# Kernel optimization log

Measured on AMD Instinct MI355X. Metric: run time of the kernel, lower is better.

## Reference

```python
import jax, jax.numpy as jnp
import numpy as np

FIX_SCALE = np.array([[0.,0.,0.],[1.,0.,0.],[0.,1.,0.],[0.,0.,1.],[-1.,0.,0.],[0.,-1.,0.]], dtype=np.float32)
NUM_HEADS = 8
ATTN_DIMS = 512
HEAD_DIMS = ATTN_DIMS // NUM_HEADS
NUM_LEARN = 6
SIG_CLAMP = 9.21  # safe_sigmoid clamp


def quat_to_rotmat(q):
    # q: [G,4] (w,x,y,z), normalized -> [G,3,3]
    q = q / jnp.linalg.norm(q, axis=-1, keepdims=True)
    w, x, y, z = q[..., 0], q[..., 1], q[..., 2], q[..., 3]
    r0 = jnp.stack([1 - 2*(y*y + z*z), 2*(x*y - w*z), 2*(x*z + w*y)], -1)
    r1 = jnp.stack([2*(x*y + w*z), 1 - 2*(x*x + z*z), 2*(y*z - w*x)], -1)
    r2 = jnp.stack([2*(x*z - w*y), 2*(y*z + w*x), 1 - 2*(x*x + y*y)], -1)
    return jnp.stack([r0, r1, r2], -2)


def bilinear_sample(fm, gx, gy):
    # fm: [C,H,W]; gx,gy: [...] in [-1,1]; align_corners=False, zero padding
    C, H, W = fm.shape
    x = (gx + 1.0) * (W * 0.5) - 0.5
    y = (gy + 1.0) * (H * 0.5) - 0.5
    x0 = jnp.floor(x); y0 = jnp.floor(y)
    wx1 = x - x0; wx0 = 1.0 - wx1
    wy1 = y - y0; wy0 = 1.0 - wy1

    def gather(xf, yf):
        xi = xf.astype(jnp.int32); yi = yf.astype(jnp.int32)
        valid = (xi >= 0) & (xi < W) & (yi >= 0) & (yi < H)
        xi = jnp.clip(xi, 0, W - 1); yi = jnp.clip(yi, 0, H - 1)
        return fm[:, yi, xi] * valid[None].astype(fm.dtype)  # [C, ...]

    out = (gather(x0, y0) * (wx0 * wy0)[None]
           + gather(x0 + 1, y0) * (wx1 * wy0)[None]
           + gather(x0, y0 + 1) * (wx0 * wy1)[None]
           + gather(x0 + 1, y0 + 1) * (wx1 * wy1)[None])
    return jnp.moveaxis(out, 0, -1)  # [..., C]


def setup_inputs() -> dict:
    key = jax.random.key(0)
    ks = jax.random.split(key, 16)
    G, BS, GFD = 8192, 1, 32
    means = jax.random.uniform(ks[0], (G, 3), minval=-1.0, maxval=1.0)
    means = means.at[:, 2].add(3.0)  # push in front of camera
    scales = jax.random.uniform(ks[1], (G, 3), minval=0.01, maxval=0.1)
    rotations = jax.random.normal(ks[2], (G, 4))
    features = jax.random.normal(ks[3], (BS, G, 3, GFD))
    transforms = jnp.tile(jnp.eye(4)[None], (G, 1, 1)) + 0.01 * jax.random.normal(ks[4], (G, 4, 4))
    f = 64.0
    proj = jnp.array([[f, 0., 32., 0.], [0., f, 32., 0.], [0., 0., 1., 0.], [0., 0., 0., 1.]], dtype=jnp.float32)
    projection = jnp.tile(proj[None], (BS, 1, 1))
    image_features = jax.random.normal(ks[5], (BS, 256, 64, 64))
    s = lambda d: 1.0 / np.sqrt(d)
    Wq = jax.random.normal(ks[6], (GFD, ATTN_DIMS)) * s(GFD)
    Wk = jax.random.normal(ks[7], (ATTN_DIMS, 256)) * s(256)
    Wv = jax.random.normal(ks[8], (ATTN_DIMS, 256)) * s(256)
    W_off = jax.random.normal(ks[9], (HEAD_DIMS + 3, NUM_LEARN * 3)) * s(HEAD_DIMS + 3)
    b_off = jnp.zeros((NUM_LEARN * 3,))
    Wout = jax.random.normal(ks[10], (ATTN_DIMS, GFD)) * s(ATTN_DIMS)
    b_out = jnp.zeros((GFD,))
    return {"means": means, "scales": scales, "rotations": rotations, "features": features,
            "transforms": transforms, "projection": projection, "image_features": image_features,
            "Wq": Wq, "Wk": Wk, "Wv": Wv, "W_off": W_off, "b_off": b_off, "Wout": Wout, "b_out": b_out}


def reference(means, scales, rotations, features, transforms, projection, image_features,
              Wq, Wk, Wv, W_off, b_off, Wout, b_out):
    G = means.shape[0]
    bs = features.shape[0]
    H, HD = NUM_HEADS, HEAD_DIMS
    h_img, w_img = image_features.shape[-2:]

    # queries: [bs,G,3,attn] -> [bs,H,G,3,hd]
    q_full = jnp.einsum('bgtf,fa->bgta', features, Wq)
    q = q_full.reshape(bs, G, 3, H, HD).transpose(0, 3, 1, 2, 4)

    # transform means to world space with per-gaussian 4x4
    homo = jnp.concatenate([means, jnp.ones((G, 1), means.dtype)], -1)  # [G,4]
    means_w = jnp.einsum('gij,gj->gi', transforms, homo)[:, :3]  # [G,3]

    # OffsetNet: per-head learnable offsets from (world mean, token-mean query)
    q_mean = q.mean(axis=3)  # [bs,H,G,hd]
    m_b = jnp.broadcast_to(means_w[None, None], (bs, H, G, 3))
    off_in = jnp.concatenate([m_b, q_mean], -1)  # [bs,H,G,hd+3]
    learnable = jax.nn.sigmoid(jnp.clip(off_in @ W_off + b_off, -SIG_CLAMP, SIG_CLAMP))
    learnable = learnable.reshape(bs, H, G, NUM_LEARN, 3) - 0.5
    fix = jnp.broadcast_to(jnp.asarray(FIX_SCALE)[None, None, None], (bs, H, G, FIX_SCALE.shape[0], 3))
    scale_all = jnp.concatenate([fix, learnable], axis=-2)  # [bs,H,G,K,3]
    K = scale_all.shape[-2]

    offset_pts = scale_all * scales[None, None, :, None, :]
    RT = jnp.swapaxes(quat_to_rotmat(rotations), -1, -2)  # [G,3,3]
    offset_pts = jnp.einsum('gij,bhgkj->bhgki', RT, offset_pts) + means_w[None, None, :, None, :]

    # project to 2D, normalize to [0,1), then to grid coords [-1,1]
    pts4 = jnp.concatenate([offset_pts, jnp.ones_like(offset_pts[..., :1])], -1)
    p = jnp.einsum('bij,bhgkj->bhgki', projection, pts4)
    p2 = p[..., :2] / jnp.clip(p[..., 2:3], 1e-5)
    wh = jnp.array([w_img, h_img], dtype=p2.dtype)
    pnorm = jnp.clip(p2 / wh, 0.0, 0.9999)
    grid = 2.0 * pnorm - 1.0  # [bs,H,G,K,2]

    # key/value maps via 1x1 conv, split into per-head channel groups
    kmap = jnp.einsum('ac,bchw->bahw', Wk, image_features).reshape(bs, H, HD, h_img, w_img)
    vmap_ = jnp.einsum('ac,bchw->bahw', Wv, image_features).reshape(bs, H, HD, h_img, w_img)

    sample_bh = jax.vmap(jax.vmap(bilinear_sample, in_axes=(0, 0, 0)), in_axes=(0, 0, 0))
    k_s = sample_bh(kmap, grid[..., 0], grid[..., 1])   # [bs,H,G,K,hd]
    v_s = sample_bh(vmap_, grid[..., 0], grid[..., 1])  # [bs,H,G,K,hd]

    scale = HD ** -0.5
    scores = jnp.einsum('bhgid,bhgkd->bhgik', q, k_s) * scale
    attn = jax.nn.softmax(scores, axis=-1)
    out = jnp.einsum('bhgik,bhgkd->bhgid', attn, v_s)  # [bs,H,G,3,hd]
    out = out.transpose(0, 2, 3, 1, 4).reshape(bs, G, 3, H * HD)  # b g i (h d)
    out = out @ Wout + b_out
    return out + features
```

## Files before the change

kernel.cpp:

```cpp
#include <hip/hip_runtime.h>
#include <hip/hip_bf16.h>

typedef __hip_bfloat16 bf16;
typedef __attribute__((ext_vector_type(8))) short short8;
typedef __attribute__((ext_vector_type(4))) float float4v;

__device__ __forceinline__ unsigned short f2bfu(float f) {
    bf16 b = __float2bfloat16(f);
    return *(unsigned short*)&b;
}
__device__ __forceinline__ void ld8bf(const bf16* p, float* f) {
    uint4 u = *(const uint4*)p;
    f[0] = __uint_as_float(u.x << 16); f[1] = __uint_as_float(u.x & 0xffff0000u);
    f[2] = __uint_as_float(u.y << 16); f[3] = __uint_as_float(u.y & 0xffff0000u);
    f[4] = __uint_as_float(u.z << 16); f[5] = __uint_as_float(u.z & 0xffff0000u);
    f[6] = __uint_as_float(u.w << 16); f[7] = __uint_as_float(u.w & 0xffff0000u);
}
__device__ __forceinline__ unsigned packbf(float lo, float hi) {
    return (unsigned)f2bfu(lo) | ((unsigned)f2bfu(hi) << 16);
}

__global__ __launch_bounds__(256) void preconvert_kernel(
    const float* __restrict__ img, const float* __restrict__ Wk,
    const float* __restrict__ Wv, unsigned short* __restrict__ imgbf,
    unsigned short* __restrict__ wkvbf)
{
    const size_t base = ((size_t)blockIdx.x * 256 + threadIdx.x) * 4;
    float4 v;
    unsigned short* dst;
    if (base < 1048576) {
        v = *(const float4*)(img + base);
        dst = imgbf + base;
    } else {
        size_t o = base - 1048576;
        v = *(const float4*)((o < 131072) ? (Wk + o) : (Wv + (o - 131072)));
        dst = wkvbf + o;
    }
    *(uint2*)dst = make_uint2(packbf(v.x, v.y), packbf(v.z, v.w));
}

__global__ __launch_bounds__(256) void conv_bf16_kernel(
    const unsigned short* __restrict__ imgbf, const unsigned short* __restrict__ wkvbf,
    bf16* __restrict__ buf)
{
    __shared__ __attribute__((aligned(16))) unsigned short Bt[64][264];
    const int tid = threadIdx.x;
    const int p0 = blockIdx.x * 64;
    const int o0 = blockIdx.y * 64;

#pragma unroll
    for (int i = 0; i < 4; i++) {
        int chunk = i * 256 + tid;
        int kp  = chunk >> 3;
        int pxg = (chunk & 7) * 8;
        uint4 r0 = *(const uint4*)(imgbf + (size_t)(2 * kp) * 4096 + p0 + pxg);
        uint4 r1 = *(const uint4*)(imgbf + (size_t)(2 * kp + 1) * 4096 + p0 + pxg);
        unsigned lo[8], hi[8];
        lo[0] = r0.x & 0xffffu; lo[1] = r0.x >> 16; lo[2] = r0.y & 0xffffu; lo[3] = r0.y >> 16;
        lo[4] = r0.z & 0xffffu; lo[5] = r0.z >> 16; lo[6] = r0.w & 0xffffu; lo[7] = r0.w >> 16;
        hi[0] = r1.x & 0xffffu; hi[1] = r1.x >> 16; hi[2] = r1.y & 0xffffu; hi[3] = r1.y >> 16;
        hi[4] = r1.z & 0xffffu; hi[5] = r1.z >> 16; hi[6] = r1.w & 0xffffu; hi[7] = r1.w >> 16;
#pragma unroll
        for (int j = 0; j < 8; j++)
            *(unsigned*)&Bt[pxg + j][2 * kp] = lo[j] | (hi[j] << 16);
    }
    __syncthreads();

    const int w = tid >> 6, l = tid & 63;
    const int m = l & 15, quad = l >> 4;
    const int mrow = w * 16 + m;
    const unsigned short* Wsel = wkvbf + ((o0 < 512) ? 0 : 131072);
    const int obase = (o0 < 512) ? o0 : (o0 - 512);

    float4v acc[4] = {{0,0,0,0},{0,0,0,0},{0,0,0,0},{0,0,0,0}};
#pragma unroll
    for (int kk = 0; kk < 8; kk++) {
        const int kofs = kk * 32 + quad * 8;
        short8 af = *(const short8*)&Bt[mrow][kofs];
#pragma unroll
        for (int nt = 0; nt < 4; nt++) {
            const int row = obase + nt * 16 + m;
            short8 b8 = *(const short8*)(Wsel + (size_t)row * 256 + kofs);
            acc[nt] = __builtin_amdgcn_mfma_f32_16x16x32_bf16(af, b8, acc[nt], 0, 0, 0);
        }
    }
#pragma unroll
    for (int nt = 0; nt < 4; nt++) {
#pragma unroll
        for (int r = 0; r < 4; r++) {
            size_t px = p0 + w * 16 + quad * 4 + r;
            buf[px * 1024 + o0 + nt * 16 + m] = __float2bfloat16(acc[nt][r]);
        }
    }
}

__global__ __launch_bounds__(256) void conv_mfma_kernel(
    const float* __restrict__ img, const float* __restrict__ Wk,
    const float* __restrict__ Wv, bf16* __restrict__ buf)
{
    __shared__ __attribute__((aligned(16))) unsigned short Bt[64][264];
    const int tid = threadIdx.x;
    const int p0 = blockIdx.x * 64;
    const int o0 = blockIdx.y * 64;

#pragma unroll
    for (int i = 0; i < 4; i++) {
        int chunk = i * 256 + tid;
        int kp  = chunk >> 3;
        int pxg = (chunk & 7) * 8;
        const float* r0 = img + (size_t)(2 * kp) * 4096 + p0 + pxg;
        const float* r1 = img + (size_t)(2 * kp + 1) * 4096 + p0 + pxg;
        float4 a0 = *(const float4*)r0, a1 = *(const float4*)(r0 + 4);
        float4 b0 = *(const float4*)r1, b1 = *(const float4*)(r1 + 4);
        unsigned lo[8], hi[8];
        lo[0] = f2bfu(a0.x); lo[1] = f2bfu(a0.y); lo[2] = f2bfu(a0.z); lo[3] = f2bfu(a0.w);
        lo[4] = f2bfu(a1.x); lo[5] = f2bfu(a1.y); lo[6] = f2bfu(a1.z); lo[7] = f2bfu(a1.w);
        hi[0] = f2bfu(b0.x); hi[1] = f2bfu(b0.y); hi[2] = f2bfu(b0.z); hi[3] = f2bfu(b0.w);
        hi[4] = f2bfu(b1.x); hi[5] = f2bfu(b1.y); hi[6] = f2bfu(b1.z); hi[7] = f2bfu(b1.w);
#pragma unroll
        for (int j = 0; j < 8; j++)
            *(unsigned*)&Bt[pxg + j][2 * kp] = lo[j] | (hi[j] << 16);
    }
    __syncthreads();

    const int w = tid >> 6, l = tid & 63;
    const int m = l & 15, quad = l >> 4;
    const int mrow = w * 16 + m;
    const float* Wsel = (o0 < 512) ? Wk : Wv;
    const int obase = (o0 < 512) ? o0 : (o0 - 512);

    float4v acc[4] = {{0,0,0,0},{0,0,0,0},{0,0,0,0},{0,0,0,0}};
#pragma unroll
    for (int kk = 0; kk < 8; kk++) {
        const int kofs = kk * 32 + quad * 8;
        short8 af = *(const short8*)&Bt[mrow][kofs];
#pragma unroll
        for (int nt = 0; nt < 4; nt++) {
            const int row = obase + nt * 16 + m;
            const float* wp = Wsel + (size_t)row * 256 + kofs;
            float4 w0 = *(const float4*)wp, w1 = *(const float4*)(wp + 4);
            short8 b8;
            b8[0] = (short)f2bfu(w0.x); b8[1] = (short)f2bfu(w0.y);
            b8[2] = (short)f2bfu(w0.z); b8[3] = (short)f2bfu(w0.w);
            b8[4] = (short)f2bfu(w1.x); b8[5] = (short)f2bfu(w1.y);
            b8[6] = (short)f2bfu(w1.z); b8[7] = (short)f2bfu(w1.w);
            acc[nt] = __builtin_amdgcn_mfma_f32_16x16x32_bf16(af, b8, acc[nt], 0, 0, 0);
        }
    }
#pragma unroll
    for (int nt = 0; nt < 4; nt++) {
#pragma unroll
        for (int r = 0; r < 4; r++) {
            size_t px = p0 + w * 16 + quad * 4 + r;
            buf[px * 1024 + o0 + nt * 16 + m] = __float2bfloat16(acc[nt][r]);
        }
    }
}

__global__ __launch_bounds__(256) void qgemm_kernel(
    const float* __restrict__ features, const float* __restrict__ Wq,
    bf16* __restrict__ qfull)
{
    __shared__ __attribute__((aligned(16))) unsigned short WqT[256][40];
    const int tid = threadIdx.x;
    const int R0 = blockIdx.x * 64;
    const int n0 = blockIdx.y * 256;
#pragma unroll
    for (int k = 0; k < 32; k++)
        WqT[tid][k] = f2bfu(Wq[(size_t)k * 512 + n0 + tid]);
    __syncthreads();

    const int w = tid >> 6, l = tid & 63, m = l & 15, quad = l >> 4;
    const int row = R0 + w * 16 + m;
    const float* fp = features + (size_t)row * 32 + quad * 8;
    float4 f0 = *(const float4*)fp, f1 = *(const float4*)(fp + 4);
    short8 af;
    af[0] = (short)f2bfu(f0.x); af[1] = (short)f2bfu(f0.y);
    af[2] = (short)f2bfu(f0.z); af[3] = (short)f2bfu(f0.w);
    af[4] = (short)f2bfu(f1.x); af[5] = (short)f2bfu(f1.y);
    af[6] = (short)f2bfu(f1.z); af[7] = (short)f2bfu(f1.w);
    float4v acc[16];
#pragma unroll
    for (int t = 0; t < 16; t++) acc[t] = (float4v){0.f, 0.f, 0.f, 0.f};
#pragma unroll
    for (int t = 0; t < 16; t++) {
        short8 b8 = *(const short8*)&WqT[t * 16 + m][quad * 8];
        acc[t] = __builtin_amdgcn_mfma_f32_16x16x32_bf16(af, b8, acc[t], 0, 0, 0);
    }
    const int rb = R0 + w * 16 + quad * 4;
#pragma unroll
    for (int t = 0; t < 16; t++)
#pragma unroll
        for (int r = 0; r < 4; r++)
            qfull[(size_t)(rb + r) * 512 + n0 + t * 16 + m] = __float2bfloat16(acc[t][r]);
}

__global__ __launch_bounds__(256, 7) void attn_core_kernel(
    const float* __restrict__ means, const float* __restrict__ scales,
    const float* __restrict__ rot,   const float* __restrict__ transforms,
    const float* __restrict__ projection, const float* __restrict__ W_off,
    const float* __restrict__ b_off, const bf16* __restrict__ buf,
    bf16* __restrict__ qfull)
{
    __shared__ __attribute__((aligned(16))) float qf[1536];
    __shared__ __attribute__((aligned(16))) unsigned short vsh[6144];
    __shared__ __attribute__((aligned(16))) float qm_u[512];
    __shared__ float lrn[144];
    __shared__ float mw[3], sc3[3], Rt[9], pr[12];

    short4* corner = (short4*)qm_u;
    float*  att    = qm_u + 192;
    float*  wofl   = (float*)vsh;
    float*  bofl   = wofl + 1206;

    const int g = blockIdx.x, tid = threadIdx.x;

    for (int i = tid; i < 1206; i += 256) wofl[i] = W_off[i];
    if (tid < 18) bofl[tid] = b_off[tid];
    if (tid >= 32 && tid < 35) {
        sc3[tid - 32] = scales[(size_t)g * 3 + (tid - 32)];
    } else if (tid >= 36 && tid < 48) {
        pr[tid - 36] = projection[tid - 36];
    } else if (tid == 48) {
        float w = rot[(size_t)g * 4],     x = rot[(size_t)g * 4 + 1];
        float y = rot[(size_t)g * 4 + 2], z = rot[(size_t)g * 4 + 3];
        float n = rsqrtf(w * w + x * x + y * y + z * z);
        w *= n; x *= n; y *= n; z *= n;
        float R00 = 1 - 2 * (y * y + z * z), R01 = 2 * (x * y - w * z), R02 = 2 * (x * z + w * y);
        float R10 = 2 * (x * y + w * z), R11 = 1 - 2 * (x * x + z * z), R12 = 2 * (y * z - w * x);
        float R20 = 2 * (x * z - w * y), R21 = 2 * (y * z + w * x), R22 = 1 - 2 * (x * x + y * y);
        Rt[0] = R00; Rt[1] = R10; Rt[2] = R20;
        Rt[3] = R01; Rt[4] = R11; Rt[5] = R21;
        Rt[6] = R02; Rt[7] = R12; Rt[8] = R22;
    } else if (tid >= 52 && tid < 55) {
        int i = tid - 52;
        float m0 = means[(size_t)g * 3];
        float m1 = means[(size_t)g * 3 + 1];
        float m2 = means[(size_t)g * 3 + 2];
        const float* T = transforms + (size_t)g * 16 + i * 4;
        mw[i] = T[0] * m0 + T[1] * m1 + T[2] * m2 + T[3];
    }
    {
        const unsigned* qsrc = (const unsigned*)((const unsigned short*)qfull + (size_t)g * 1536);
#pragma unroll
        for (int i = 0; i < 3; i++) {
            int e = tid + i * 256;
            unsigned u = qsrc[e];
            qf[e * 2]     = __uint_as_float(u << 16);
            qf[e * 2 + 1] = __uint_as_float(u & 0xffff0000u);
        }
    }
    __syncthreads();

    qm_u[tid]       = (qf[tid]       + qf[tid + 512] + qf[tid + 1024]) * (1.f / 3.f);
    qm_u[tid + 256] = (qf[tid + 256] + qf[tid + 768] + qf[tid + 1280]) * (1.f / 3.f);
    __syncthreads();

    if (tid < 144) {
        int h = tid / 18, l = tid % 18;
        float s = bofl[l];
#pragma unroll
        for (int i = 0; i < 3; i++) s += mw[i] * wofl[i * 18 + l];
        for (int d = 0; d < 64; d++) s += qm_u[h * 64 + d] * wofl[(3 + d) * 18 + l];
        s = fminf(fmaxf(s, -9.21f), 9.21f);
        lrn[tid] = 1.f / (1.f + expf(-s)) - 0.5f;
    }
    __syncthreads();

    if (tid < 96) {
        int h = tid / 12, k = tid % 12;
        float s0, s1, s2;
        if (k < 6) {
            const float FSx[6] = {0.f, 1.f, 0.f, 0.f, -1.f, 0.f};
            const float FSy[6] = {0.f, 0.f, 1.f, 0.f, 0.f, -1.f};
            const float FSz[6] = {0.f, 0.f, 0.f, 1.f, 0.f, 0.f};
            s0 = FSx[k]; s1 = FSy[k]; s2 = FSz[k];
        } else {
            int b = h * 18 + (k - 6) * 3;
            s0 = lrn[b]; s1 = lrn[b + 1]; s2 = lrn[b + 2];
        }
        float o0 = s0 * sc3[0], o1 = s1 * sc3[1], o2 = s2 * sc3[2];
        float wx = Rt[0] * o0 + Rt[1] * o1 + Rt[2] * o2 + mw[0];
        float wy = Rt[3] * o0 + Rt[4] * o1 + Rt[5] * o2 + mw[1];
        float wz = Rt[6] * o0 + Rt[7] * o1 + Rt[8] * o2 + mw[2];
        float px = pr[0] * wx + pr[1] * wy + pr[2]  * wz + pr[3];
        float py = pr[4] * wx + pr[5] * wy + pr[6]  * wz + pr[7];
        float pz = pr[8] * wx + pr[9] * wy + pr[10] * wz + pr[11];
        pz = fmaxf(pz, 1e-5f);
        float gx = fminf(fmaxf(px / pz * (1.f / 64.f), 0.f), 0.9999f);
        float gy = fminf(fmaxf(py / pz * (1.f / 64.f), 0.f), 0.9999f);
        float x = gx * 64.f - 0.5f, y = gy * 64.f - 0.5f;
        float fx = floorf(x), fy = floorf(y);
        short4 cn;
        cn.x = (short)(int)fx;
        cn.y = (short)(int)fy;
        cn.z = (short)(unsigned short)fminf((x - fx) * 65536.f, 65535.f);
        cn.w = (short)(unsigned short)fminf((y - fy) * 65536.f, 65535.f);
        corner[tid] = cn;
    }
    __syncthreads();

    {
        const int slice = tid & 7, d0 = slice * 8, grp = tid >> 3;
#pragma unroll
        for (int it = 0; it < 3; it++) {
            const int p = it * 32 + grp;
            const int h = p / 12, k = p - h * 12;
            short4 cn = corner[p];
            int x0 = cn.x, y0 = cn.y, x1 = x0 + 1, y1 = y0 + 1;
            float wx1 = (float)(unsigned short)cn.z * (1.f / 65536.f);
            float wy1 = (float)(unsigned short)cn.w * (1.f / 65536.f);
            float wx0 = 1.f - wx1, wy0 = 1.f - wy1;
            bool vx0 = (unsigned)x0 < 64u, vx1 = (unsigned)x1 < 64u;
            bool vy0 = (unsigned)y0 < 64u, vy1 = (unsigned)y1 < 64u;
            int xc0 = min(max(x0, 0), 63), xc1 = min(max(x1, 0), 63);
            int yc0 = min(max(y0, 0), 63), yc1 = min(max(y1, 0), 63);
            int   off[4];
            float wt[4];
            off[0] = (yc0 * 64 + xc0) * 1024; wt[0] = (vx0 & vy0) ? wx0 * wy0 : 0.f;
            off[1] = (yc0 * 64 + xc1) * 1024; wt[1] = (vx1 & vy0) ? wx1 * wy0 : 0.f;
            off[2] = (yc1 * 64 + xc0) * 1024; wt[2] = (vx0 & vy1) ? wx0 * wy1 : 0.f;
            off[3] = (yc1 * 64 + xc1) * 1024; wt[3] = (vx1 & vy1) ? wx1 * wy1 : 0.f;
            const int a = h * 64 + d0;
            const bf16* bp = buf + a;
            float ka[8] = {0,0,0,0,0,0,0,0}, va[8] = {0,0,0,0,0,0,0,0}, t8[8];
#pragma unroll
            for (int c = 0; c < 4; c++) {
                const float w = wt[c];
                ld8bf(bp + off[c], t8);
#pragma unroll
                for (int j = 0; j < 8; j++) ka[j] += w * t8[j];
                ld8bf(bp + off[c] + 512, t8);
#pragma unroll
                for (int j = 0; j < 8; j++) va[j] += w * t8[j];
            }
            uint4 pv;
            pv.x = packbf(va[0], va[1]); pv.y = packbf(va[2], va[3]);
            pv.z = packbf(va[4], va[5]); pv.w = packbf(va[6], va[7]);
            *(uint4*)(vsh + p * 64 + d0) = pv;
            float sp[3];
#pragma unroll
            for (int t = 0; t < 3; t++) {
                const float* qp = qf + t * 512 + a;
                float s = 0.f;
#pragma unroll
                for (int j = 0; j < 8; j++) s += qp[j] * ka[j];
                sp[t] = s;
            }
#pragma unroll
            for (int msk = 1; msk < 8; msk <<= 1) {
#pragma unroll
                for (int t = 0; t < 3; t++) sp[t] += __shfl_xor(sp[t], msk);
            }
            if (slice == 0) {
#pragma unroll
                for (int t = 0; t < 3; t++) att[(h * 3 + t) * 12 + k] = sp[t] * 0.125f;
            }
        }
    }
    __syncthreads();

    if (tid < 24) {
        float* row = att + tid * 12;
        float m = row[0];
#pragma unroll
        for (int k = 1; k < 12; k++) m = fmaxf(m, row[k]);
        float e_[12]; float ssum = 0.f;
#pragma unroll
        for (int k = 0; k < 12; k++) { e_[k] = expf(row[k] - m); ssum += e_[k]; }
        float inv = 1.f / ssum;
#pragma unroll
        for (int k = 0; k < 12; k++) row[k] = e_[k] * inv;
    }
    __syncthreads();

    {
        unsigned* oa32 = (unsigned*)((unsigned short*)qfull + (size_t)g * 1536);
#pragma unroll
        for (int i = 0; i < 3; i++) {
            int e = tid + i * 256;
            int t = e >> 8, a2 = (e & 255) * 2;
            int h = a2 >> 6, dd = a2 & 63;
            const float* ar = att + (h * 3 + t) * 12;
            const unsigned short* vp = vsh + (h * 12) * 64 + dd;
            float s0 = 0.f, s1 = 0.f;
#pragma unroll
            for (int k = 0; k < 12; k++) {
                unsigned u = *(const unsigned*)(vp + k * 64);
                s0 += ar[k] * __uint_as_float(u << 16);
                s1 += ar[k] * __uint_as_float(u & 0xffff0000u);
            }
            oa32[e] = packbf(s0, s1);
        }
    }
}

__global__ __launch_bounds__(256) void outgemm_kernel(
    const bf16* __restrict__ oa, const float* __restrict__ Wout,
    const float* __restrict__ b_out, const float* __restrict__ features,
    float* __restrict__ out)
{
    __shared__ __attribute__((aligned(16))) unsigned short WT[32][520];
    const int tid = threadIdx.x;
    const int R0 = blockIdx.x * 64;
#pragma unroll
    for (int j = 0; j < 64; j++) {
        int lin = j * 256 + tid;
        WT[lin & 31][lin >> 5] = f2bfu(Wout[lin]);
    }
    __syncthreads();

    const int w = tid >> 6, l = tid & 63, m = l & 15, quad = l >> 4;
    const int row = R0 + w * 16 + m;
    float4v acc[2] = {{0,0,0,0},{0,0,0,0}};
#pragma unroll
    for (int kk = 0; kk < 16; kk++) {
        short8 af = *(const short8*)((const unsigned short*)oa + (size_t)row * 512 + kk * 32 + quad * 8);
#pragma unroll
        for (int t = 0; t < 2; t++) {
            short8 b8 = *(const short8*)&WT[t * 16 + m][kk * 32 + quad * 8];
            acc[t] = __builtin_amdgcn_mfma_f32_16x16x32_bf16(af, b8, acc[t], 0, 0, 0);
        }
    }
    const int rb = R0 + w * 16 + quad * 4;
#pragma unroll
    for (int t = 0; t < 2; t++) {
        int col = t * 16 + m;
        float bb = b_out[col];
#pragma unroll
        for (int r = 0; r < 4; r++) {
            int rr = rb + r;
            out[(size_t)rr * 32 + col] = acc[t][r] + bb + features[(size_t)rr * 32 + col];
        }
    }
}

__global__ __launch_bounds__(256, 6) void attn_fused_kernel(
    const float* __restrict__ means, const float* __restrict__ scales,
    const float* __restrict__ rot,   const float* __restrict__ features,
    const float* __restrict__ transforms, const float* __restrict__ projection,
    const float* __restrict__ Wq,    const float* __restrict__ W_off,
    const float* __restrict__ b_off, const float* __restrict__ Wout,
    const float* __restrict__ b_out, const bf16* __restrict__ buf,
    float* __restrict__ out)
{
    __shared__ float feat[96];
    __shared__ __attribute__((aligned(16))) float qf[1536];
    __shared__ float qm[512];
    __shared__ float mw[3], sc3[3], Rt[9], pr[12];
    __shared__ float lrn[144];
    __shared__ int   coff[96][4];
    __shared__ float cwt[96][4];
    __shared__ __attribute__((aligned(16))) char pool[12288];
    __shared__ float att[288];

    unsigned short* vsh = (unsigned short*)pool;
    const int g = blockIdx.x, tid = threadIdx.x;

    if (tid < 96) {
        feat[tid] = features[(size_t)g * 96 + tid];
    } else if (tid < 99) {
        sc3[tid - 96] = scales[(size_t)g * 3 + (tid - 96)];
    } else if (tid >= 100 && tid < 112) {
        pr[tid - 100] = projection[tid - 100];
    } else if (tid == 112) {
        float w = rot[(size_t)g * 4],     x = rot[(size_t)g * 4 + 1];
        float y = rot[(size_t)g * 4 + 2], z = rot[(size_t)g * 4 + 3];
        float n = rsqrtf(w * w + x * x + y * y + z * z);
        w *= n; x *= n; y *= n; z *= n;
        float R00 = 1 - 2 * (y * y + z * z), R01 = 2 * (x * y - w * z), R02 = 2 * (x * z + w * y);
        float R10 = 2 * (x * y + w * z), R11 = 1 - 2 * (x * x + z * z), R12 = 2 * (y * z - w * x);
        float R20 = 2 * (x * z - w * y), R21 = 2 * (y * z + w * x), R22 = 1 - 2 * (x * x + y * y);
        Rt[0] = R00; Rt[1] = R10; Rt[2] = R20;
        Rt[3] = R01; Rt[4] = R11; Rt[5] = R21;
        Rt[6] = R02; Rt[7] = R12; Rt[8] = R22;
    } else if (tid >= 116 && tid < 119) {
        int i = tid - 116;
        float m0 = means[(size_t)g * 3];
        float m1 = means[(size_t)g * 3 + 1];
        float m2 = means[(size_t)g * 3 + 2];
        const float* T = transforms + (size_t)g * 16 + i * 4;
        mw[i] = T[0] * m0 + T[1] * m1 + T[2] * m2 + T[3];
    }
    __syncthreads();

    {
        const int a0 = tid * 2;
        float s00 = 0.f, s01 = 0.f, s10 = 0.f, s11 = 0.f, s20 = 0.f, s21 = 0.f;
#pragma unroll
        for (int f = 0; f < 32; f++) {
            float2 w2 = *(const float2*)(Wq + (size_t)f * 512 + a0);
            float f0 = feat[f], f1 = feat[32 + f], f2 = feat[64 + f];
            s00 += f0 * w2.x; s01 += f0 * w2.y;
            s10 += f1 * w2.x; s11 += f1 * w2.y;
            s20 += f2 * w2.x; s21 += f2 * w2.y;
        }
        *(float2*)(qf + a0)        = make_float2(s00, s01);
        *(float2*)(qf + 512 + a0)  = make_float2(s10, s11);
        *(float2*)(qf + 1024 + a0) = make_float2(s20, s21);
    }
    __syncthreads();

    qm[tid]       = (qf[tid]       + qf[tid + 512] + qf[tid + 1024]) * (1.f / 3.f);
    qm[tid + 256] = (qf[tid + 256] + qf[tid + 768] + qf[tid + 1280]) * (1.f / 3.f);
    __syncthreads();

    if (tid < 144) {
        int h = tid / 18, l = tid % 18;
        float s = b_off[l];
#pragma unroll
        for (int i = 0; i < 3; i++) s += mw[i] * W_off[i * 18 + l];
        for (int d = 0; d < 64; d++) s += qm[h * 64 + d] * W_off[(size_t)(3 + d) * 18 + l];
        s = fminf(fmaxf(s, -9.21f), 9.21f);
        lrn[tid] = 1.f / (1.f + expf(-s)) - 0.5f;
    }
    __syncthreads();

    if (tid < 96) {
        int h = tid / 12, k = tid % 12;
        float s0, s1, s2;
        if (k < 6) {
            const float FSx[6] = {0.f, 1.f, 0.f, 0.f, -1.f, 0.f};
            const float FSy[6] = {0.f, 0.f, 1.f, 0.f, 0.f, -1.f};
            const float FSz[6] = {0.f, 0.f, 0.f, 1.f, 0.f, 0.f};
            s0 = FSx[k]; s1 = FSy[k]; s2 = FSz[k];
        } else {
            int b = h * 18 + (k - 6) * 3;
            s0 = lrn[b]; s1 = lrn[b + 1]; s2 = lrn[b + 2];
        }
        float o0 = s0 * sc3[0], o1 = s1 * sc3[1], o2 = s2 * sc3[2];
        float wx = Rt[0] * o0 + Rt[1] * o1 + Rt[2] * o2 + mw[0];
        float wy = Rt[3] * o0 + Rt[4] * o1 + Rt[5] * o2 + mw[1];
        float wz = Rt[6] * o0 + Rt[7] * o1 + Rt[8] * o2 + mw[2];
        float px = pr[0] * wx + pr[1] * wy + pr[2]  * wz + pr[3];
        float py = pr[4] * wx + pr[5] * wy + pr[6]  * wz + pr[7];
        float pz = pr[8] * wx + pr[9] * wy + pr[10] * wz + pr[11];
        pz = fmaxf(pz, 1e-5f);
        float gx = fminf(fmaxf(px / pz * (1.f / 64.f), 0.f), 0.9999f);
        float gy = fminf(fmaxf(py / pz * (1.f / 64.f), 0.f), 0.9999f);
        float x = gx * 64.f - 0.5f, y = gy * 64.f - 0.5f;
        float fx = floorf(x), fy = floorf(y);
        int x0 = (int)fx, y0 = (int)fy;
        float wx1 = x - fx, wx0c = 1.f - wx1;
        float wy1 = y - fy, wy0c = 1.f - wy1;
        int xs[2] = {x0, x0 + 1}, ys[2] = {y0, y0 + 1};
        float wxs[2] = {wx0c, wx1}, wys[2] = {wy0c, wy1};
#pragma unroll
        for (int c = 0; c < 4; c++) {
            int dx = c & 1, dy = c >> 1;
            int xi = xs[dx], yi = ys[dy];
            bool v = (xi >= 0) & (xi < 64) & (yi >= 0) & (yi < 64);
            int xc = min(max(xi, 0), 63), yc = min(max(yi, 0), 63);
            coff[tid][c] = (yc * 64 + xc) * 1024;
            cwt[tid][c]  = v ? wxs[dx] * wys[dy] : 0.f;
        }
    }
    __syncthreads();

    {
        const int slice = tid & 7, d0 = slice * 8, grp = tid >> 3;
#pragma unroll
        for (int it = 0; it < 3; it++) {
            const int p = it * 32 + grp;
            const int h = p / 12, k = p - h * 12;
            const int a = h * 64 + d0;
            const bf16* bp = buf + a;
            float ka[8] = {0,0,0,0,0,0,0,0}, va[8] = {0,0,0,0,0,0,0,0}, t8[8];
#pragma unroll
            for (int c = 0; c < 4; c++) {
                const int   o = coff[p][c];
                const float w = cwt[p][c];
                ld8bf(bp + o, t8);
#pragma unroll
                for (int j = 0; j < 8; j++) ka[j] += w * t8[j];
                ld8bf(bp + o + 512, t8);
#pragma unroll
                for (int j = 0; j < 8; j++) va[j] += w * t8[j];
            }
            uint4 pv;
            pv.x = packbf(va[0], va[1]); pv.y = packbf(va[2], va[3]);
            pv.z = packbf(va[4], va[5]); pv.w = packbf(va[6], va[7]);
            *(uint4*)(vsh + p * 64 + d0) = pv;
            float sp[3];
#pragma unroll
            for (int t = 0; t < 3; t++) {
                const float* qp = qf + t * 512 + a;
                float s = 0.f;
#pragma unroll
                for (int j = 0; j < 8; j++) s += qp[j] * ka[j];
                sp[t] = s;
            }
#pragma unroll
            for (int msk = 1; msk < 8; msk <<= 1) {
#pragma unroll
                for (int t = 0; t < 3; t++) sp[t] += __shfl_xor(sp[t], msk);
            }
            if (slice == 0) {
#pragma unroll
                for (int t = 0; t < 3; t++) att[(h * 3 + t) * 12 + k] = sp[t] * 0.125f;
            }
        }
    }
    __syncthreads();

    if (tid < 24) {
        float* row = att + tid * 12;
        float m = row[0];
#pragma unroll
        for (int k = 1; k < 12; k++) m = fmaxf(m, row[k]);
        float e_[12]; float ssum = 0.f;
#pragma unroll
        for (int k = 0; k < 12; k++) { e_[k] = expf(row[k] - m); ssum += e_[k]; }
        float inv = 1.f / ssum;
#pragma unroll
        for (int k = 0; k < 12; k++) row[k] = e_[k] * inv;
    }
    __syncthreads();

#pragma unroll
    for (int i = 0; i < 6; i++) {
        int e = tid + i * 256;
        int t = e >> 9, a = e & 511, h = a >> 6, dd = a & 63;
        const float* ar = att + (h * 3 + t) * 12;
        const unsigned short* vp = vsh + (h * 12) * 64 + dd;
        float s = 0.f;
#pragma unroll
        for (int k = 0; k < 12; k++)
            s += ar[k] * __uint_as_float((unsigned)vp[k * 64] << 16);
        qf[e] = s;
    }
    __syncthreads();

    {
        float* red = (float*)pool;
        const int c0 = (tid & 15) * 2, slice = tid >> 4;
        const int abase = slice * 32;
        float a00 = 0.f, a01 = 0.f, a10 = 0.f, a11 = 0.f, a20 = 0.f, a21 = 0.f;
#pragma unroll
        for (int i = 0; i < 32; i++) {
            int a = abase + i;
            float2 w2 = *(const float2*)(Wout + (size_t)a * 32 + c0);
            float o0 = qf[a], o1 = qf[512 + a], o2 = qf[1024 + a];
            a00 += o0 * w2.x; a01 += o0 * w2.y;
            a10 += o1 * w2.x; a11 += o1 * w2.y;
            a20 += o2 * w2.x; a21 += o2 * w2.y;
        }
        __syncthreads();
        red[(slice * 3 + 0) * 32 + c0] = a00; red[(slice * 3 + 0) * 32 + c0 + 1] = a01;
        red[(slice * 3 + 1) * 32 + c0] = a10; red[(slice * 3 + 1) * 32 + c0 + 1] = a11;
        red[(slice * 3 + 2) * 32 + c0] = a20; red[(slice * 3 + 2) * 32 + c0 + 1] = a21;
        __syncthreads();
        if (tid < 96) {
            int t = tid >> 5, c = tid & 31;
            float acc = b_out[c] + feat[tid];
#pragma unroll
            for (int s = 0; s < 16; s++) acc += red[(s * 3 + t) * 32 + c];
            out[(size_t)g * 96 + tid] = acc;
        }
    }
}

extern "C" void kernel_launch(void* const* d_in, const int* in_sizes, int n_in,
                              void* d_out, int out_size, void* d_ws, size_t ws_size,
                              hipStream_t stream) {
    const float* means      = (const float*)d_in[0];
    const float* scales     = (const float*)d_in[1];
    const float* rot        = (const float*)d_in[2];
    const float* features   = (const float*)d_in[3];
    const float* transforms = (const float*)d_in[4];
    const float* projection = (const float*)d_in[5];
    const float* img        = (const float*)d_in[6];
    const float* Wq         = (const float*)d_in[7];
    const float* Wk         = (const float*)d_in[8];
    const float* Wv         = (const float*)d_in[9];
    const float* W_off      = (const float*)d_in[10];
    const float* b_off      = (const float*)d_in[11];
    const float* Wout       = (const float*)d_in[12];
    const float* b_out      = (const float*)d_in[13];
    float* out = (float*)d_out;

    char* w = (char*)d_ws;
    bf16* buf = (bf16*)(w + 64);
    const size_t BUF_BYTES = (size_t)4096 * 1024 * 2;
    const size_t Q_BYTES   = (size_t)24576 * 512 * 2;
    const size_t need = 64 + BUF_BYTES + Q_BYTES;

    dim3 gridc(64, 16);
    if (ws_size >= need) {
        bf16* qfull = (bf16*)(w + 64 + BUF_BYTES);
        unsigned short* imgbf = (unsigned short*)qfull;
        unsigned short* wkvbf = imgbf + 1048576;
        preconvert_kernel<<<1280, 256, 0, stream>>>(img, Wk, Wv, imgbf, wkvbf);
        conv_bf16_kernel<<<gridc, 256, 0, stream>>>(imgbf, wkvbf, buf);
        dim3 gridq(384, 2);
        qgemm_kernel<<<gridq, 256, 0, stream>>>(features, Wq, qfull);
        attn_core_kernel<<<8192, 256, 0, stream>>>(
            means, scales, rot, transforms, projection, W_off, b_off, buf, qfull);
        outgemm_kernel<<<384, 256, 0, stream>>>(qfull, Wout, b_out, features, out);
    } else {
        conv_mfma_kernel<<<gridc, 256, 0, stream>>>(img, Wk, Wv, buf);
        attn_fused_kernel<<<8192, 256, 0, stream>>>(
            means, scales, rot, features, transforms, projection,
            Wq, W_off, b_off, Wout, b_out, buf, out);
    }
}
```

Measured before the change: 183.8 us.

## Switch intermediate storage and MFMA paths from bf16 to fp16 with packed math

Converts all intermediate buffers (conv output, q, attention output) from bf16 to fp16 and uses fp16 MFMA. In the attention core it keeps q in shared memory as packed half2, does the bilinear gather accumulation with packed half2 FMAs and the score dot products with fdot2. It also accumulates the value weighting in half2. Halving the shared-memory footprint for q lets launch bounds rise from 7 to 8 blocks per CU. The cost is fp16 range and precision risk, especially when accumulating in half precision.

```diff
diff --git a/kernel.cpp b/kernel.cpp
--- a/kernel.cpp
+++ b/kernel.cpp
@@ -1,47 +1,48 @@
 #include <hip/hip_runtime.h>
 #include <hip/hip_bf16.h>
-
-typedef __hip_bfloat16 bf16;
-typedef __attribute__((ext_vector_type(8))) short short8;
+#include <hip/hip_fp16.h>
+
+typedef _Float16 half2v __attribute__((ext_vector_type(2)));
+typedef _Float16 half8v __attribute__((ext_vector_type(8)));
 typedef __attribute__((ext_vector_type(4))) float float4v;
 
-__device__ __forceinline__ unsigned short f2bfu(float f) {
-    bf16 b = __float2bfloat16(f);
-    return *(unsigned short*)&b;
-}
-__device__ __forceinline__ void ld8bf(const bf16* p, float* f) {
+__device__ __forceinline__ half2v u2h(unsigned u) { return __builtin_bit_cast(half2v, u); }
+__device__ __forceinline__ unsigned h2u(half2v h) { return __builtin_bit_cast(unsigned, h); }
+__device__ __forceinline__ unsigned short f2hu(float f) {
+    _Float16 h = (_Float16)f; return __builtin_bit_cast(unsigned short, h);
+}
+__device__ __forceinline__ unsigned packh(float lo, float hi) {
+    half2v h; h[0] = (_Float16)lo; h[1] = (_Float16)hi; return h2u(h);
+}
+__device__ __forceinline__ void ld8h(const unsigned short* p, float* f) {
     uint4 u = *(const uint4*)p;
-    f[0] = __uint_as_float(u.x << 16); f[1] = __uint_as_float(u.x & 0xffff0000u);
-    f[2] = __uint_as_float(u.y << 16); f[3] = __uint_as_float(u.y & 0xffff0000u);
-    f[4] = __uint_as_float(u.z << 16); f[5] = __uint_as_float(u.z & 0xffff0000u);
-    f[6] = __uint_as_float(u.w << 16); f[7] = __uint_as_float(u.w & 0xffff0000u);
-}
-__device__ __forceinline__ unsigned packbf(float lo, float hi) {
-    return (unsigned)f2bfu(lo) | ((unsigned)f2bfu(hi) << 16);
+    half2v h0 = u2h(u.x), h1 = u2h(u.y), h2 = u2h(u.z), h3 = u2h(u.w);
+    f[0] = (float)h0[0]; f[1] = (float)h0[1]; f[2] = (float)h1[0]; f[3] = (float)h1[1];
+    f[4] = (float)h2[0]; f[5] = (float)h2[1]; f[6] = (float)h3[0]; f[7] = (float)h3[1];
 }
 
 __global__ __launch_bounds__(256) void preconvert_kernel(
     const float* __restrict__ img, const float* __restrict__ Wk,
-    const float* __restrict__ Wv, unsigned short* __restrict__ imgbf,
-    unsigned short* __restrict__ wkvbf)
+    const float* __restrict__ Wv, unsigned short* __restrict__ imgh,
+    unsigned short* __restrict__ wkvh)
 {
     const size_t base = ((size_t)blockIdx.x * 256 + threadIdx.x) * 4;
     float4 v;
     unsigned short* dst;
     if (base < 1048576) {
         v = *(const float4*)(img + base);
-        dst = imgbf + base;
+        dst = imgh + base;
     } else {
         size_t o = base - 1048576;
         v = *(const float4*)((o < 131072) ? (Wk + o) : (Wv + (o - 131072)));
-        dst = wkvbf + o;
-    }
-    *(uint2*)dst = make_uint2(packbf(v.x, v.y), packbf(v.z, v.w));
-}
-
-__global__ __launch_bounds__(256) void conv_bf16_kernel(
-    const unsigned short* __restrict__ imgbf, const unsigned short* __restrict__ wkvbf,
-    bf16* __restrict__ buf)
+        dst = wkvh + o;
+    }
+    *(uint2*)dst = make_uint2(packh(v.x, v.y), packh(v.z, v.w));
+}
+
+__global__ __launch_bounds__(256) void conv_f16_kernel(
+    const unsigned short* __restrict__ imgh, const unsigned short* __restrict__ wkvh,
+    unsigned short* __restrict__ buf)
 {
     __shared__ __attribute__((aligned(16))) unsigned short Bt[64][264];
     const int tid = threadIdx.x;
@@ -53,8 +54,8 @@
         int chunk = i * 256 + tid;
         int kp  = chunk >> 3;
         int pxg = (chunk & 7) * 8;
-        uint4 r0 = *(const uint4*)(imgbf + (size_t)(2 * kp) * 4096 + p0 + pxg);
-        uint4 r1 = *(const uint4*)(imgbf + (size_t)(2 * kp + 1) * 4096 + p0 + pxg);
+        uint4 r0 = *(const uint4*)(imgh + (size_t)(2 * kp) * 4096 + p0 + pxg);
+        uint4 r1 = *(const uint4*)(imgh + (size_t)(2 * kp + 1) * 4096 + p0 + pxg);
         unsigned lo[8], hi[8];
         lo[0] = r0.x & 0xffffu; lo[1] = r0.x >> 16; lo[2] = r0.y & 0xffffu; lo[3] = r0.y >> 16;
         lo[4] = r0.z & 0xffffu; lo[5] = r0.z >> 16; lo[6] = r0.w & 0xffffu; lo[7] = r0.w >> 16;
@@ -69,19 +70,19 @@
     const int w = tid >> 6, l = tid & 63;
     const int m = l & 15, quad = l >> 4;
     const int mrow = w * 16 + m;
-    const unsigned short* Wsel = wkvbf + ((o0 < 512) ? 0 : 131072);
+    const unsigned short* Wsel = wkvh + ((o0 < 512) ? 0 : 131072);
     const int obase = (o0 < 512) ? o0 : (o0 - 512);
 
     float4v acc[4] = {{0,0,0,0},{0,0,0,0},{0,0,0,0},{0,0,0,0}};
 #pragma unroll
     for (int kk = 0; kk < 8; kk++) {
         const int kofs = kk * 32 + quad * 8;
-        short8 af = *(const short8*)&Bt[mrow][kofs];
+        half8v af = *(const half8v*)&Bt[mrow][kofs];
 #pragma unroll
         for (int nt = 0; nt < 4; nt++) {
             const int row = obase + nt * 16 + m;
-            short8 b8 = *(const short8*)(Wsel + (size_t)row * 256 + kofs);
-            acc[nt] = __builtin_amdgcn_mfma_f32_16x16x32_bf16(af, b8, acc[nt], 0, 0, 0);
+            half8v b8 = *(const half8v*)(Wsel + (size_t)row * 256 + kofs);
+            acc[nt] = __builtin_amdgcn_mfma_f32_16x16x32_f16(af, b8, acc[nt], 0, 0, 0);
         }
     }
 #pragma unroll
@@ -89,14 +90,14 @@
 #pragma unroll
         for (int r = 0; r < 4; r++) {
             size_t px = p0 + w * 16 + quad * 4 + r;
-            buf[px * 1024 + o0 + nt * 16 + m] = __float2bfloat16(acc[nt][r]);
+            buf[px * 1024 + o0 + nt * 16 + m] = f2hu(acc[nt][r]);
         }
     }
 }
 
 __global__ __launch_bounds__(256) void conv_mfma_kernel(
     const float* __restrict__ img, const float* __restrict__ Wk,
-    const float* __restrict__ Wv, bf16* __restrict__ buf)
+    const float* __restrict__ Wv, unsigned short* __restrict__ buf)
 {
     __shared__ __attribute__((aligned(16))) unsigned short Bt[64][264];
     const int tid = threadIdx.x;
@@ -113,10 +114,10 @@
         float4 a0 = *(const float4*)r0, a1 = *(const float4*)(r0 + 4);
         float4 b0 = *(const float4*)r1, b1 = *(const float4*)(r1 + 4);
         unsigned lo[8], hi[8];
-        lo[0] = f2bfu(a0.x); lo[1] = f2bfu(a0.y); lo[2] = f2bfu(a0.z); lo[3] = f2bfu(a0.w);
-        lo[4] = f2bfu(a1.x); lo[5] = f2bfu(a1.y); lo[6] = f2bfu(a1.z); lo[7] = f2bfu(a1.w);
-        hi[0] = f2bfu(b0.x); hi[1] = f2bfu(b0.y); hi[2] = f2bfu(b0.z); hi[3] = f2bfu(b0.w);
-        hi[4] = f2bfu(b1.x); hi[5] = f2bfu(b1.y); hi[6] = f2bfu(b1.z); hi[7] = f2bfu(b1.w);
+        lo[0] = f2hu(a0.x); lo[1] = f2hu(a0.y); lo[2] = f2hu(a0.z); lo[3] = f2hu(a0.w);
+        lo[4] = f2hu(a1.x); lo[5] = f2hu(a1.y); lo[6] = f2hu(a1.z); lo[7] = f2hu(a1.w);
+        hi[0] = f2hu(b0.x); hi[1] = f2hu(b0.y); hi[2] = f2hu(b0.z); hi[3] = f2hu(b0.w);
+        hi[4] = f2hu(b1.x); hi[5] = f2hu(b1.y); hi[6] = f2hu(b1.z); hi[7] = f2hu(b1.w);
 #pragma unroll
         for (int j = 0; j < 8; j++)
             *(unsigned*)&Bt[pxg + j][2 * kp] = lo[j] | (hi[j] << 16);
@@ -133,18 +134,18 @@
 #pragma unroll
     for (int kk = 0; kk < 8; kk++) {
         const int kofs = kk * 32 + quad * 8;
-        short8 af = *(const short8*)&Bt[mrow][kofs];
+        half8v af = *(const half8v*)&Bt[mrow][kofs];
 #pragma unroll
         for (int nt = 0; nt < 4; nt++) {
             const int row = obase + nt * 16 + m;
             const float* wp = Wsel + (size_t)row * 256 + kofs;
             float4 w0 = *(const float4*)wp, w1 = *(const float4*)(wp + 4);
-            short8 b8;
-            b8[0] = (short)f2bfu(w0.x); b8[1] = (short)f2bfu(w0.y);
-            b8[2] = (short)f2bfu(w0.z); b8[3] = (short)f2bfu(w0.w);
-            b8[4] = (short)f2bfu(w1.x); b8[5] = (short)f2bfu(w1.y);
-            b8[6] = (short)f2bfu(w1.z); b8[7] = (short)f2bfu(w1.w);
-            acc[nt] = __builtin_amdgcn_mfma_f32_16x16x32_bf16(af, b8, acc[nt], 0, 0, 0);
+            half8v b8;
+            b8[0] = (_Float16)w0.x; b8[1] = (_Float16)w0.y;
+            b8[2] = (_Float16)w0.z; b8[3] = (_Float16)w0.w;
+            b8[4] = (_Float16)w1.x; b8[5] = (_Float16)w1.y;
+            b8[6] = (_Float16)w1.z; b8[7] = (_Float16)w1.w;
+            acc[nt] = __builtin_amdgcn_mfma_f32_16x16x32_f16(af, b8, acc[nt], 0, 0, 0);
         }
     }
 #pragma unroll
@@ -152,14 +153,14 @@
 #pragma unroll
         for (int r = 0; r < 4; r++) {
             size_t px = p0 + w * 16 + quad * 4 + r;
-            buf[px * 1024 + o0 + nt * 16 + m] = __float2bfloat16(acc[nt][r]);
+            buf[px * 1024 + o0 + nt * 16 + m] = f2hu(acc[nt][r]);
         }
     }
 }
 
 __global__ __launch_bounds__(256) void qgemm_kernel(
     const float* __restrict__ features, const float* __restrict__ Wq,
-    bf16* __restrict__ qfull)
+    unsigned short* __restrict__ qfull)
 {
     __shared__ __attribute__((aligned(16))) unsigned short WqT[256][40];
     const int tid = threadIdx.x;
@@ -167,50 +168,50 @@
     const int n0 = blockIdx.y * 256;
 #pragma unroll
     for (int k = 0; k < 32; k++)
-        WqT[tid][k] = f2bfu(Wq[(size_t)k * 512 + n0 + tid]);
+        WqT[tid][k] = f2hu(Wq[(size_t)k * 512 + n0 + tid]);
     __syncthreads();
 
     const int w = tid >> 6, l = tid & 63, m = l & 15, quad = l >> 4;
     const int row = R0 + w * 16 + m;
     const float* fp = features + (size_t)row * 32 + quad * 8;
     float4 f0 = *(const float4*)fp, f1 = *(const float4*)(fp + 4);
-    short8 af;
-    af[0] = (short)f2bfu(f0.x); af[1] = (short)f2bfu(f0.y);
-    af[2] = (short)f2bfu(f0.z); af[3] = (short)f2bfu(f0.w);
-    af[4] = (short)f2bfu(f1.x); af[5] = (short)f2bfu(f1.y);
-    af[6] = (short)f2bfu(f1.z); af[7] = (short)f2bfu(f1.w);
+    half8v af;
+    af[0] = (_Float16)f0.x; af[1] = (_Float16)f0.y;
+    af[2] = (_Float16)f0.z; af[3] = (_Float16)f0.w;
+    af[4] = (_Float16)f1.x; af[5] = (_Float16)f1.y;
+    af[6] = (_Float16)f1.z; af[7] = (_Float16)f1.w;
     float4v acc[16];
 #pragma unroll
     for (int t = 0; t < 16; t++) acc[t] = (float4v){0.f, 0.f, 0.f, 0.f};
 #pragma unroll
     for (int t = 0; t < 16; t++) {
-        short8 b8 = *(const short8*)&WqT[t * 16 + m][quad * 8];
-        acc[t] = __builtin_amdgcn_mfma_f32_16x16x32_bf16(af, b8, acc[t], 0, 0, 0);
+        half8v b8 = *(const half8v*)&WqT[t * 16 + m][quad * 8];
+        acc[t] = __builtin_amdgcn_mfma_f32_16x16x32_f16(af, b8, acc[t], 0, 0, 0);
     }
     const int rb = R0 + w * 16 + quad * 4;
 #pragma unroll
     for (int t = 0; t < 16; t++)
 #pragma unroll
         for (int r = 0; r < 4; r++)
-            qfull[(size_t)(rb + r) * 512 + n0 + t * 16 + m] = __float2bfloat16(acc[t][r]);
-}
-
-__global__ __launch_bounds__(256, 7) void attn_core_kernel(
+            qfull[(size_t)(rb + r) * 512 + n0 + t * 16 + m] = f2hu(acc[t][r]);
+}
+
+__global__ __launch_bounds__(256, 8) void attn_core_kernel(
     const float* __restrict__ means, const float* __restrict__ scales,
     const float* __restrict__ rot,   const float* __restrict__ transforms,
     const float* __restrict__ projection, const float* __restrict__ W_off,
-    const float* __restrict__ b_off, const bf16* __restrict__ buf,
-    bf16* __restrict__ qfull)
+    const float* __restrict__ b_off, const unsigned short* __restrict__ buf,
+    unsigned short* __restrict__ qfull)
 {
-    __shared__ __attribute__((aligned(16))) float qf[1536];
-    __shared__ __attribute__((aligned(16))) unsigned short vsh[6144];
+    __shared__ __attribute__((aligned(16))) unsigned qf2[768];
+    __shared__ __attribute__((aligned(16))) unsigned vsh2[3072];
     __shared__ __attribute__((aligned(16))) float qm_u[512];
     __shared__ float lrn[144];
     __shared__ float mw[3], sc3[3], Rt[9], pr[12];
 
     short4* corner = (short4*)qm_u;
     float*  att    = qm_u + 192;
-    float*  wofl   = (float*)vsh;
+    float*  wofl   = (float*)vsh2;
     float*  bofl   = wofl + 1206;
 
     const int g = blockIdx.x, tid = threadIdx.x;
@@ -241,19 +242,20 @@
         mw[i] = T[0] * m0 + T[1] * m1 + T[2] * m2 + T[3];
     }
     {
-        const unsigned* qsrc = (const unsigned*)((const unsigned short*)qfull + (size_t)g * 1536);
+        const unsigned* qsrc = (const unsigned*)(qfull + (size_t)g * 1536);
 #pragma unroll
         for (int i = 0; i < 3; i++) {
             int e = tid + i * 256;
-            unsigned u = qsrc[e];
-            qf[e * 2]     = __uint_as_float(u << 16);
-            qf[e * 2 + 1] = __uint_as_float(u & 0xffff0000u);
-        }
-    }
-    __syncthreads();
-
-    qm_u[tid]       = (qf[tid]       + qf[tid + 512] + qf[tid + 1024]) * (1.f / 3.f);
-    qm_u[tid + 256] = (qf[tid + 256] + qf[tid + 768] + qf[tid + 1280]) * (1.f / 3.f);
+            qf2[e] = qsrc[e];
+        }
+    }
+    __syncthreads();
+
+    {
+        half2v a = u2h(qf2[tid]), b = u2h(qf2[256 + tid]), c = u2h(qf2[512 + tid]);
+        qm_u[tid * 2]     = ((float)a[0] + (float)b[0] + (float)c[0]) * (1.f / 3.f);
+        qm_u[tid * 2 + 1] = ((float)a[1] + (float)b[1] + (float)c[1]) * (1.f / 3.f);
+    }
     __syncthreads();
 
     if (tid < 144) {
@@ -301,7 +303,7 @@
     __syncthreads();
 
     {
-        const int slice = tid & 7, d0 = slice * 8, grp = tid >> 3;
+        const int slice = tid & 7, grp = tid >> 3;
 #pragma unroll
         for (int it = 0; it < 3; it++) {
             const int p = it * 32 + grp;
@@ -321,30 +323,32 @@
             off[1] = (yc0 * 64 + xc1) * 1024; wt[1] = (vx1 & vy0) ? wx1 * wy0 : 0.f;
             off[2] = (yc1 * 64 + xc0) * 1024; wt[2] = (vx0 & vy1) ? wx0 * wy1 : 0.f;
             off[3] = (yc1 * 64 + xc1) * 1024; wt[3] = (vx1 & vy1) ? wx1 * wy1 : 0.f;
-            const int a = h * 64 + d0;
-            const bf16* bp = buf + a;
-            float ka[8] = {0,0,0,0,0,0,0,0}, va[8] = {0,0,0,0,0,0,0,0}, t8[8];
+            const int a = h * 64 + slice * 8;
+            const unsigned short* bp = buf + a;
+            half2v ka2[4] = {{0,0},{0,0},{0,0},{0,0}};
+            half2v va2[4] = {{0,0},{0,0},{0,0},{0,0}};
 #pragma unroll
             for (int c = 0; c < 4; c++) {
-                const float w = wt[c];
-                ld8bf(bp + off[c], t8);
-#pragma unroll
-                for (int j = 0; j < 8; j++) ka[j] += w * t8[j];
-                ld8bf(bp + off[c] + 512, t8);
-#pragma unroll
-                for (int j = 0; j < 8; j++) va[j] += w * t8[j];
-            }
-            uint4 pv;
-            pv.x = packbf(va[0], va[1]); pv.y = packbf(va[2], va[3]);
-            pv.z = packbf(va[4], va[5]); pv.w = packbf(va[6], va[7]);
-            *(uint4*)(vsh + p * 64 + d0) = pv;
+                _Float16 wh = (_Float16)wt[c];
+                half2v w2; w2[0] = wh; w2[1] = wh;
+                uint4 uk = *(const uint4*)(bp + off[c]);
+                uint4 uv = *(const uint4*)(bp + off[c] + 512);
+                ka2[0] += w2 * u2h(uk.x); ka2[1] += w2 * u2h(uk.y);
+                ka2[2] += w2 * u2h(uk.z); ka2[3] += w2 * u2h(uk.w);
+                va2[0] += w2 * u2h(uv.x); va2[1] += w2 * u2h(uv.y);
+                va2[2] += w2 * u2h(uv.z); va2[3] += w2 * u2h(uv.w);
+            }
+            const int pa = h * 32 + slice * 4;
+            *(uint4*)&vsh2[p * 32 + slice * 4] =
+                make_uint4(h2u(va2[0]), h2u(va2[1]), h2u(va2[2]), h2u(va2[3]));
             float sp[3];
 #pragma unroll
             for (int t = 0; t < 3; t++) {
-                const float* qp = qf + t * 512 + a;
-                float s = 0.f;
-#pragma unroll
-                for (int j = 0; j < 8; j++) s += qp[j] * ka[j];
+                uint4 q4 = *(const uint4*)&qf2[t * 256 + pa];
+                float s = __builtin_amdgcn_fdot2(u2h(q4.x), ka2[0], 0.f, false);
+                s = __builtin_amdgcn_fdot2(u2h(q4.y), ka2[1], s, false);
+                s = __builtin_amdgcn_fdot2(u2h(q4.z), ka2[2], s, false);
+                s = __builtin_amdgcn_fdot2(u2h(q4.w), ka2[3], s, false);
                 sp[t] = s;
             }
 #pragma unroll
@@ -375,28 +379,28 @@
     __syncthreads();
 
     {
-        unsigned* oa32 = (unsigned*)((unsigned short*)qfull + (size_t)g * 1536);
+        unsigned* oa32 = (unsigned*)(qfull + (size_t)g * 1536);
 #pragma unroll
         for (int i = 0; i < 3; i++) {
             int e = tid + i * 256;
-            int t = e >> 8, a2 = (e & 255) * 2;
-            int h = a2 >> 6, dd = a2 & 63;
+            int t = e >> 8, a2p = e & 255;
+            int h = a2p >> 5, ddp = a2p & 31;
             const float* ar = att + (h * 3 + t) * 12;
-            const unsigned short* vp = vsh + (h * 12) * 64 + dd;
-            float s0 = 0.f, s1 = 0.f;
+            const unsigned* vp = vsh2 + h * 12 * 32 + ddp;
+            half2v acc = {0, 0};
 #pragma unroll
             for (int k = 0; k < 12; k++) {
-                unsigned u = *(const unsigned*)(vp + k * 64);
-                s0 += ar[k] * __uint_as_float(u << 16);
-                s1 += ar[k] * __uint_as_float(u & 0xffff0000u);
-            }
-            oa32[e] = packbf(s0, s1);
+                _Float16 ah = (_Float16)ar[k];
+                half2v a2; a2[0] = ah; a2[1] = ah;
+                acc += a2 * u2h(vp[k * 32]);
+            }
+            oa32[e] = h2u(acc);
         }
     }
 }
 
 __global__ __launch_bounds__(256) void outgemm_kernel(
-    const bf16* __restrict__ oa, const float* __restrict__ Wout,
+    const unsigned short* __restrict__ oa, const float* __restrict__ Wout,
     const float* __restrict__ b_out, const float* __restrict__ features,
     float* __restrict__ out)
 {
@@ -406,7 +410,7 @@
 #pragma unroll
     for (int j = 0; j < 64; j++) {
         int lin = j * 256 + tid;
-        WT[lin & 31][lin >> 5] = f2bfu(Wout[lin]);
+        WT[lin & 31][lin >> 5] = f2hu(Wout[lin]);
     }
     __syncthreads();
 
@@ -415,11 +419,11 @@
     float4v acc[2] = {{0,0,0,0},{0,0,0,0}};
 #pragma unroll
     for (int kk = 0; kk < 16; kk++) {
-        short8 af = *(const short8*)((const unsigned short*)oa + (size_t)row * 512 + kk * 32 + quad * 8);
+        half8v af = *(const half8v*)(oa + (size_t)row * 512 + kk * 32 + quad * 8);
 #pragma unroll
         for (int t = 0; t < 2; t++) {
-            short8 b8 = *(const short8*)&WT[t * 16 + m][kk * 32 + quad * 8];
-            acc[t] = __builtin_amdgcn_mfma_f32_16x16x32_bf16(af, b8, acc[t], 0, 0, 0);
+            half8v b8 = *(const half8v*)&WT[t * 16 + m][kk * 32 + quad * 8];
+            acc[t] = __builtin_amdgcn_mfma_f32_16x16x32_f16(af, b8, acc[t], 0, 0, 0);
         }
     }
     const int rb = R0 + w * 16 + quad * 4;
@@ -441,7 +445,7 @@
     const float* __restrict__ transforms, const float* __restrict__ projection,
     const float* __restrict__ Wq,    const float* __restrict__ W_off,
     const float* __restrict__ b_off, const float* __restrict__ Wout,
-    const float* __restrict__ b_out, const bf16* __restrict__ buf,
+    const float* __restrict__ b_out, const unsigned short* __restrict__ buf,
     float* __restrict__ out)
 {
     __shared__ float feat[96];
@@ -564,22 +568,22 @@
             const int p = it * 32 + grp;
             const int h = p / 12, k = p - h * 12;
             const int a = h * 64 + d0;
-            const bf16* bp = buf + a;
+            const unsigned short* bp = buf + a;
             float ka[8] = {0,0,0,0,0,0,0,0}, va[8] = {0,0,0,0,0,0,0,0}, t8[8];
 #pragma unroll
             for (int c = 0; c < 4; c++) {
                 const int   o = coff[p][c];
                 const float w = cwt[p][c];
-                ld8bf(bp + o, t8);
+                ld8h(bp + o, t8);
 #pragma unroll
                 for (int j = 0; j < 8; j++) ka[j] += w * t8[j];
-                ld8bf(bp + o + 512, t8);
+                ld8h(bp + o + 512, t8);
 #pragma unroll
                 for (int j = 0; j < 8; j++) va[j] += w * t8[j];
             }
             uint4 pv;
-            pv.x = packbf(va[0], va[1]); pv.y = packbf(va[2], va[3]);
-            pv.z = packbf(va[4], va[5]); pv.w = packbf(va[6], va[7]);
+            pv.x = packh(va[0], va[1]); pv.y = packh(va[2], va[3]);
+            pv.z = packh(va[4], va[5]); pv.w = packh(va[6], va[7]);
             *(uint4*)(vsh + p * 64 + d0) = pv;
             float sp[3];
 #pragma unroll
@@ -625,8 +629,10 @@
         const unsigned short* vp = vsh + (h * 12) * 64 + dd;
         float s = 0.f;
 #pragma unroll
-        for (int k = 0; k < 12; k++)
-            s += ar[k] * __uint_as_float((unsigned)vp[k * 64] << 16);
+        for (int k = 0; k < 12; k++) {
+            _Float16 hh = __builtin_bit_cast(_Float16, vp[k * 64]);
+            s += ar[k] * (float)hh;
+        }
         qf[e] = s;
     }
     __syncthreads();
@@ -680,18 +686,18 @@
     float* out = (float*)d_out;
 
     char* w = (char*)d_ws;
-    bf16* buf = (bf16*)(w + 64);
+    unsigned short* buf = (unsigned short*)(w + 64);
     const size_t BUF_BYTES = (size_t)4096 * 1024 * 2;
     const size_t Q_BYTES   = (size_t)24576 * 512 * 2;
     const size_t need = 64 + BUF_BYTES + Q_BYTES;
 
     dim3 gridc(64, 16);
     if (ws_size >= need) {
-        bf16* qfull = (bf16*)(w + 64 + BUF_BYTES);
-        unsigned short* imgbf = (unsigned short*)qfull;
-        unsigned short* wkvbf = imgbf + 1048576;
-        preconvert_kernel<<<1280, 256, 0, stream>>>(img, Wk, Wv, imgbf, wkvbf);
-        conv_bf16_kernel<<<gridc, 256, 0, stream>>>(imgbf, wkvbf, buf);
+        unsigned short* qfull = (unsigned short*)(w + 64 + BUF_BYTES);
+        unsigned short* imgh = qfull;
+        unsigned short* wkvh = imgh + 1048576;
+        preconvert_kernel<<<1280, 256, 0, stream>>>(img, Wk, Wv, imgh, wkvh);
+        conv_f16_kernel<<<gridc, 256, 0, stream>>>(imgh, wkvh, buf);
         dim3 gridq(384, 2);
         qgemm_kernel<<<gridq, 256, 0, stream>>>(features, Wq, qfull);
         attn_core_kernel<<<8192, 256, 0, stream>>>(
```

Result: faster. 174.5 us (-5.1%).
